# Kernel optimization log

Hardware: AMD Instinct MI355X
Metric: run time of the kernel (lower is better)

The kernel has to match this reference:

```python
import jax, jax.numpy as jnp
import numpy as np

N_NODES = 1024
FEAT = 64
NEG_BIG = -9e15

def setup_inputs() -> dict:
    key = jax.random.key(0)
    ks = jax.random.split(key, 12)
    B, S, D = 4, 16384, FEAT
    flow_features = jax.random.normal(ks[0], (B, S, D), dtype=jnp.float32)
    src_ips = jax.random.randint(ks[1], (B, S), 0, N_NODES)
    dst_ips = jax.random.randint(ks[2], (B, S), 0, N_NODES)
    flow_volumes = jax.random.uniform(ks[3], (B, S), dtype=jnp.float32) * 2000.0
    emb = jax.random.normal(ks[4], (N_NODES, D), dtype=jnp.float32) * 0.02
    We1 = jax.random.normal(ks[5], (2 * D, 32), dtype=jnp.float32) * 0.1
    be1 = jnp.zeros((32,), dtype=jnp.float32)
    We2 = jax.random.normal(ks[6], (32, 1), dtype=jnp.float32) * 0.1
    be2 = jnp.zeros((1,), dtype=jnp.float32)
    W = jax.random.normal(ks[7], (D, D), dtype=jnp.float32) * 0.1
    a1 = jax.random.normal(ks[8], (D,), dtype=jnp.float32) * 0.1
    a2 = jax.random.normal(ks[9], (D,), dtype=jnp.float32) * 0.1
    return dict(flow_features=flow_features, src_ips=src_ips, dst_ips=dst_ips,
                flow_volumes=flow_volumes, emb=emb, We1=We1, be1=be1, We2=We2,
                be2=be2, W=W, a1=a1, a2=a2)

def _forward(flow_features, flow_volumes, emb, We1, be1, We2, be2, W, a1, a2,
             src_ips, dst_ips):
    B, S, D = flow_features.shape
    N = emb.shape[0]
    # --- DynamicGraphBuilder: scatter-add flow features at dst nodes ---
    node = jax.vmap(lambda f, d: jnp.zeros((N, D), f.dtype).at[d].add(f))(
        flow_features, dst_ips)                         # (B, N, D)
    nrm = jnp.maximum(jnp.linalg.norm(node, axis=-1, keepdims=True), 1e-12)
    h = node / nrm                                      # F.normalize(p=2)
    # --- edge weights: MLP over concat(src_emb, dst_emb), scaled by volume ---
    pair = jnp.concatenate([emb[src_ips], emb[dst_ips]], axis=-1)  # (B, S, 2D)
    mid = jax.nn.relu(pair @ We1 + be1)
    ew = jax.nn.sigmoid((mid @ We2 + be2)[..., 0])      # (B, S)
    w = ew * jax.nn.sigmoid(flow_volumes / 1000.0)
    adj = jax.vmap(lambda s, d, ww: jnp.zeros((N, N), ww.dtype)
                   .at[s, d].set(ww).at[d, s].set(ww))(src_ips, dst_ips, w)
    # --- GraphAttentionLayer (decomposed e_ij = a1.Wh_i + a2.Wh_j) ---
    Wh = h @ W                                          # (B, N, D)
    f1 = Wh @ a1                                        # (B, N)
    f2 = Wh @ a2                                        # (B, N)
    e = jax.nn.leaky_relu(f1[:, :, None] + f2[:, None, :], 0.2)  # (B, N, N)
    attn = jax.nn.softmax(jnp.where(adj > 0, e, NEG_BIG), axis=-1)
    return jax.nn.elu(jnp.einsum('bij,bjd->bid', attn, Wh))       # (B, N, D)

def reference(flow_features, src_ips, dst_ips, flow_volumes, emb, We1, be1,
              We2, be2, W, a1, a2):
    return _forward(flow_features, flow_volumes, emb, We1, be1, We2, be2,
                    W, a1, a2, src_ips, dst_ips)
```

## Files before the change

kernel.cpp:

```cpp
#include <hip/hip_runtime.h>
#include <math.h>

#define BB 4
#define SS 16384
#define NN 1024
#define DD 64
#define MW 32
#define CAP 256
#define JCAP 256

__device__ __forceinline__ float wave_sum(float v) {
    #pragma unroll
    for (int off = 32; off > 0; off >>= 1) v += __shfl_xor(v, off, 64);
    return v;
}
__device__ __forceinline__ float wave_max(float v) {
    #pragma unroll
    for (int off = 32; off > 0; off >>= 1) v = fmaxf(v, __shfl_xor(v, off, 64));
    return v;
}

__global__ __launch_bounds__(256) void build_kernel(
        const int* __restrict__ src_ips, const int* __restrict__ dst_ips,
        int* __restrict__ count, int* __restrict__ bucket,
        unsigned int* __restrict__ mask) {
    int tid = blockIdx.x * 256 + threadIdx.x;
    int b   = tid >> 14;
    int dst = dst_ips[tid];
    int src = src_ips[tid];
    int row = (b << 10) + dst;
    int pos = atomicAdd(count + row, 1);
    if (pos < CAP) bucket[row * CAP + pos] = tid;
    unsigned int* mb = mask + (size_t)b * NN * MW;
    atomicOr(mb + src * MW + (dst >> 5), 1u << (dst & 31));
    atomicOr(mb + dst * MW + (src >> 5), 1u << (src & 31));
}

__global__ __launch_bounds__(256) void gather_transform_kernel(
        const float* __restrict__ ff, const int* __restrict__ count,
        const int* __restrict__ bucket, const float* __restrict__ W,
        const float* __restrict__ a1, const float* __restrict__ a2,
        float* __restrict__ Wh, float* __restrict__ f1, float* __restrict__ f2) {
    __shared__ float Ws[DD * DD];
    __shared__ float hs[4][DD];
    __shared__ float a1s[DD], a2s[DD];
    int t = threadIdx.x;
    for (int i = t; i < DD * DD / 4; i += 256)
        ((float4*)Ws)[i] = ((const float4*)W)[i];
    if (t < DD) { a1s[t] = a1[t]; a2s[t] = a2[t]; }
    int wave = t >> 6, lane = t & 63;
    int fq = lane >> 4;
    int qi = lane & 15;
    int row = blockIdx.x * 4 + wave;

    int cnt = min(count[row], CAP);
    const int* bk = bucket + (size_t)row * CAP;
    int bkreg = (lane < cnt) ? bk[lane] : 0;
    float4 v = make_float4(0.f, 0.f, 0.f, 0.f);
    int lim = min(cnt, 64);
    for (int base = 0; base < lim; base += 4) {
        int fi = base + fq;
        int flow = __shfl(bkreg, fi, 64);
        if (fi < lim) {
            float4 x = ((const float4*)(ff + (size_t)flow * DD))[qi];
            v.x += x.x; v.y += x.y; v.z += x.z; v.w += x.w;
        }
    }
    for (int base = 64; base < cnt; base += 4) {
        int fi = base + fq;
        if (fi < cnt) {
            int flow = bk[fi];
            float4 x = ((const float4*)(ff + (size_t)flow * DD))[qi];
            v.x += x.x; v.y += x.y; v.z += x.z; v.w += x.w;
        }
    }
    #pragma unroll
    for (int off = 16; off <= 32; off <<= 1) {
        v.x += __shfl_xor(v.x, off, 64);
        v.y += __shfl_xor(v.y, off, 64);
        v.z += __shfl_xor(v.z, off, 64);
        v.w += __shfl_xor(v.w, off, 64);
    }
    float ssq = (fq == 0) ? (v.x*v.x + v.y*v.y + v.z*v.z + v.w*v.w) : 0.f;
    float nrm = fmaxf(sqrtf(wave_sum(ssq)), 1e-12f);
    float inv = 1.f / nrm;
    __syncthreads();
    if (fq == 0)
        ((float4*)hs[wave])[qi] = make_float4(v.x*inv, v.y*inv, v.z*inv, v.w*inv);
    float whl = 0.f;
    #pragma unroll
    for (int k = 0; k < DD; ++k)
        whl = fmaf(hs[wave][k], Ws[k * DD + lane], whl);
    Wh[row * DD + lane] = whl;
    float p1 = wave_sum(whl * a1s[lane]);
    float p2 = wave_sum(whl * a2s[lane]);
    if (lane == 0) { f1[row] = p1; f2[row] = p2; }
}

__global__ __launch_bounds__(256) void attn_kernel(
        const unsigned int* __restrict__ mask, const float* __restrict__ f1,
        const float* __restrict__ f2, const float* __restrict__ Wh,
        float* __restrict__ out) {
    __shared__ unsigned int ms[4][MW];
    __shared__ float ps[4][NN];
    __shared__ int   jls[4][JCAP];
    int t = threadIdx.x;
    int wave = t >> 6, lane = t & 63;
    int row = blockIdx.x * 4 + wave;
    int b = row >> 10;
    const unsigned int* mrow = mask + (size_t)row * MW;
    if (lane < MW) ms[wave][lane] = mrow[lane];
    __syncthreads();
    const float* f2b = f2 + b * NN;
    const float* Whb = Wh + (size_t)(b << 10) * DD;
    float f1i = f1[row];

    unsigned int mword = (lane < MW) ? ms[wave][lane] : 0u;
    int pc = __popc(mword);
    int x = pc;
    #pragma unroll
    for (int off = 1; off < 64; off <<= 1) {
        int y = __shfl_up(x, off, 64);
        if (lane >= off) x += y;
    }
    int cnt = __shfl(x, 63, 64);
    int o = x - pc;
    if (cnt <= JCAP) {
        unsigned int bits = mword;
        while (bits) {
            int bidx = __ffs(bits) - 1; bits &= bits - 1;
            jls[wave][o++] = (lane << 5) + bidx;
        }
    }
    __syncthreads();

    float ev[16];
    float m = -INFINITY;
    #pragma unroll
    for (int tt = 0; tt < 16; ++tt) {
        int j = lane + (tt << 6);
        ev[tt] = -INFINITY;
        if (ms[wave][j >> 5] & (1u << (j & 31))) {
            float e = f1i + f2b[j];
            ev[tt] = (e >= 0.f) ? e : 0.2f * e;
            m = fmaxf(m, ev[tt]);
        }
    }
    m = wave_max(m);
    float lsum = 0.f;
    #pragma unroll
    for (int tt = 0; tt < 16; ++tt) {
        float p = (ev[tt] > -INFINITY) ? __expf(ev[tt] - m) : 0.f;
        ps[wave][lane + (tt << 6)] = p;
        lsum += p;
    }
    lsum = wave_sum(lsum);

    float acc = 0.f;
    if (cnt > 0 && cnt <= JCAP) {
        const int* jl = jls[wave];
        int k = 0;
        for (; k + 4 <= cnt; k += 4) {
            int j0 = jl[k], j1 = jl[k+1], j2 = jl[k+2], j3 = jl[k+3];
            float w0 = Whb[j0 * DD + lane];
            float w1 = Whb[j1 * DD + lane];
            float w2 = Whb[j2 * DD + lane];
            float w3 = Whb[j3 * DD + lane];
            acc = fmaf(ps[wave][j0], w0, acc);
            acc = fmaf(ps[wave][j1], w1, acc);
            acc = fmaf(ps[wave][j2], w2, acc);
            acc = fmaf(ps[wave][j3], w3, acc);
        }
        for (; k < cnt; ++k) {
            int j = jl[k];
            acc = fmaf(ps[wave][j], Whb[j * DD + lane], acc);
        }
        acc /= lsum;
    } else if (cnt > JCAP) {
        for (int w = 0; w < MW; ++w) {
            unsigned int bits = ms[wave][w];
            while (bits) {
                int j = (w << 5) + (__ffs(bits) - 1);
                bits &= bits - 1;
                acc = fmaf(ps[wave][j], Whb[j * DD + lane], acc);
            }
        }
        acc /= lsum;
    } else {
        for (int j = 0; j < NN; ++j) acc += Whb[j * DD + lane];
        acc *= (1.f / NN);
    }
    out[row * DD + lane] = (acc > 0.f) ? acc : expm1f(acc);
}

extern "C" void kernel_launch(void* const* d_in, const int* in_sizes, int n_in,
                              void* d_out, int out_size, void* d_ws, size_t ws_size,
                              hipStream_t stream) {
    const float* ff      = (const float*)d_in[0];
    const int*   src_ips = (const int*)d_in[1];
    const int*   dst_ips = (const int*)d_in[2];
    const float* W  = (const float*)d_in[9];
    const float* a1 = (const float*)d_in[10];
    const float* a2 = (const float*)d_in[11];
    float* out = (float*)d_out;

    char* ws = (char*)d_ws;
    int* count         = (int*)ws;
    unsigned int* mask = (unsigned int*)(ws + (16 << 10));
    float* f1          = (float*)(ws + (528 << 10));
    float* f2          = (float*)(ws + (544 << 10));
    int* bucket        = (int*)(ws + (1 << 20));
    float* Wh          = (float*)(ws + (5 << 20));

    hipMemsetAsync(count, 0, (528 << 10), stream);

    build_kernel<<<BB * SS / 256, 256, 0, stream>>>(src_ips, dst_ips, count, bucket, mask);
    gather_transform_kernel<<<BB * NN / 4, 256, 0, stream>>>(ff, count, bucket, W, a1, a2, Wh, f1, f2);
    attn_kernel<<<BB * NN / 4, 256, 0, stream>>>(mask, f1, f2, Wh, out);
}
```

Measured before the change: 110.0 us.

## Compute softmax only over neighbor list and vectorize aggregation with float4 lanes

The attention kernel now computes scores, max and exp only for the compacted neighbor list instead of all 1024 columns, and stores probabilities in a small per-neighbor shared array. The weighted aggregation is reorganized so each quarter-wave handles a different neighbor, with float4 loads and a cross-quarter shuffle reduction. The mask word is kept in registers via shuffles, which removes the shared staging and both block barriers. The aim is to cut wasted exp and memory work on sparse rows, at the cost of recomputing f2 lookups twice and more code branches.

```diff
diff --git a/kernel.cpp b/kernel.cpp
--- a/kernel.cpp
+++ b/kernel.cpp
@@ -101,21 +101,17 @@
         const unsigned int* __restrict__ mask, const float* __restrict__ f1,
         const float* __restrict__ f2, const float* __restrict__ Wh,
         float* __restrict__ out) {
-    __shared__ unsigned int ms[4][MW];
-    __shared__ float ps[4][NN];
     __shared__ int   jls[4][JCAP];
+    __shared__ float pls[4][JCAP];
     int t = threadIdx.x;
     int wave = t >> 6, lane = t & 63;
     int row = blockIdx.x * 4 + wave;
     int b = row >> 10;
-    const unsigned int* mrow = mask + (size_t)row * MW;
-    if (lane < MW) ms[wave][lane] = mrow[lane];
-    __syncthreads();
+    unsigned int mword = (lane < MW) ? mask[(size_t)row * MW + lane] : 0u;
     const float* f2b = f2 + b * NN;
     const float* Whb = Wh + (size_t)(b << 10) * DD;
     float f1i = f1[row];
 
-    unsigned int mword = (lane < MW) ? ms[wave][lane] : 0u;
     int pc = __popc(mword);
     int x = pc;
     #pragma unroll
@@ -132,65 +128,117 @@
             jls[wave][o++] = (lane << 5) + bidx;
         }
     }
-    __syncthreads();
-
-    float ev[16];
-    float m = -INFINITY;
-    #pragma unroll
-    for (int tt = 0; tt < 16; ++tt) {
-        int j = lane + (tt << 6);
-        ev[tt] = -INFINITY;
-        if (ms[wave][j >> 5] & (1u << (j & 31))) {
+
+    int fq = lane >> 4;
+    int qi = lane & 15;
+
+    if (cnt > 0 && cnt <= JCAP) {
+        float m = -INFINITY;
+        for (int k = lane; k < cnt; k += 64) {
+            int j = jls[wave][k];
             float e = f1i + f2b[j];
-            ev[tt] = (e >= 0.f) ? e : 0.2f * e;
-            m = fmaxf(m, ev[tt]);
-        }
-    }
-    m = wave_max(m);
-    float lsum = 0.f;
-    #pragma unroll
-    for (int tt = 0; tt < 16; ++tt) {
-        float p = (ev[tt] > -INFINITY) ? __expf(ev[tt] - m) : 0.f;
-        ps[wave][lane + (tt << 6)] = p;
-        lsum += p;
-    }
-    lsum = wave_sum(lsum);
-
-    float acc = 0.f;
-    if (cnt > 0 && cnt <= JCAP) {
-        const int* jl = jls[wave];
-        int k = 0;
-        for (; k + 4 <= cnt; k += 4) {
-            int j0 = jl[k], j1 = jl[k+1], j2 = jl[k+2], j3 = jl[k+3];
-            float w0 = Whb[j0 * DD + lane];
-            float w1 = Whb[j1 * DD + lane];
-            float w2 = Whb[j2 * DD + lane];
-            float w3 = Whb[j3 * DD + lane];
-            acc = fmaf(ps[wave][j0], w0, acc);
-            acc = fmaf(ps[wave][j1], w1, acc);
-            acc = fmaf(ps[wave][j2], w2, acc);
-            acc = fmaf(ps[wave][j3], w3, acc);
-        }
-        for (; k < cnt; ++k) {
-            int j = jl[k];
-            acc = fmaf(ps[wave][j], Whb[j * DD + lane], acc);
-        }
-        acc /= lsum;
-    } else if (cnt > JCAP) {
+            e = (e >= 0.f) ? e : 0.2f * e;
+            m = fmaxf(m, e);
+        }
+        m = wave_max(m);
+        float lsum = 0.f;
+        for (int k = lane; k < cnt; k += 64) {
+            int j = jls[wave][k];
+            float e = f1i + f2b[j];
+            e = (e >= 0.f) ? e : 0.2f * e;
+            float p = __expf(e - m);
+            pls[wave][k] = p;
+            lsum += p;
+        }
+        lsum = wave_sum(lsum);
+        float4 acc = make_float4(0.f, 0.f, 0.f, 0.f);
+        for (int k = fq; k < cnt; k += 4) {
+            int j   = jls[wave][k];
+            float p = pls[wave][k];
+            float4 w = ((const float4*)(Whb + (size_t)j * DD))[qi];
+            acc.x = fmaf(p, w.x, acc.x);
+            acc.y = fmaf(p, w.y, acc.y);
+            acc.z = fmaf(p, w.z, acc.z);
+            acc.w = fmaf(p, w.w, acc.w);
+        }
+        #pragma unroll
+        for (int off = 16; off <= 32; off <<= 1) {
+            acc.x += __shfl_xor(acc.x, off, 64);
+            acc.y += __shfl_xor(acc.y, off, 64);
+            acc.z += __shfl_xor(acc.z, off, 64);
+            acc.w += __shfl_xor(acc.w, off, 64);
+        }
+        if (fq == 0) {
+            float inv = 1.f / lsum;
+            float4 r;
+            r.x = acc.x * inv; r.y = acc.y * inv;
+            r.z = acc.z * inv; r.w = acc.w * inv;
+            r.x = (r.x > 0.f) ? r.x : expm1f(r.x);
+            r.y = (r.y > 0.f) ? r.y : expm1f(r.y);
+            r.z = (r.z > 0.f) ? r.z : expm1f(r.z);
+            r.w = (r.w > 0.f) ? r.w : expm1f(r.w);
+            ((float4*)(out + (size_t)row * DD))[qi] = r;
+        }
+    } else if (cnt == 0) {
+        float4 acc = make_float4(0.f, 0.f, 0.f, 0.f);
+        for (int k = fq; k < NN; k += 4) {
+            float4 w = ((const float4*)(Whb + (size_t)k * DD))[qi];
+            acc.x += w.x; acc.y += w.y; acc.z += w.z; acc.w += w.w;
+        }
+        #pragma unroll
+        for (int off = 16; off <= 32; off <<= 1) {
+            acc.x += __shfl_xor(acc.x, off, 64);
+            acc.y += __shfl_xor(acc.y, off, 64);
+            acc.z += __shfl_xor(acc.z, off, 64);
+            acc.w += __shfl_xor(acc.w, off, 64);
+        }
+        if (fq == 0) {
+            float4 r;
+            r.x = acc.x * (1.f / NN); r.y = acc.y * (1.f / NN);
+            r.z = acc.z * (1.f / NN); r.w = acc.w * (1.f / NN);
+            r.x = (r.x > 0.f) ? r.x : expm1f(r.x);
+            r.y = (r.y > 0.f) ? r.y : expm1f(r.y);
+            r.z = (r.z > 0.f) ? r.z : expm1f(r.z);
+            r.w = (r.w > 0.f) ? r.w : expm1f(r.w);
+            ((float4*)(out + (size_t)row * DD))[qi] = r;
+        }
+    } else {
+        float m = -INFINITY;
+        for (int tt = 0; tt < 16; ++tt) {
+            int j = lane + (tt << 6);
+            unsigned int wv = __shfl(mword, j >> 5, 64);
+            if (wv & (1u << (j & 31))) {
+                float e = f1i + f2b[j];
+                e = (e >= 0.f) ? e : 0.2f * e;
+                m = fmaxf(m, e);
+            }
+        }
+        m = wave_max(m);
+        float lsum = 0.f;
+        for (int tt = 0; tt < 16; ++tt) {
+            int j = lane + (tt << 6);
+            unsigned int wv = __shfl(mword, j >> 5, 64);
+            if (wv & (1u << (j & 31))) {
+                float e = f1i + f2b[j];
+                e = (e >= 0.f) ? e : 0.2f * e;
+                lsum += __expf(e - m);
+            }
+        }
+        lsum = wave_sum(lsum);
+        float acc = 0.f;
         for (int w = 0; w < MW; ++w) {
-            unsigned int bits = ms[wave][w];
+            unsigned int bits = __shfl(mword, w, 64);
             while (bits) {
                 int j = (w << 5) + (__ffs(bits) - 1);
                 bits &= bits - 1;
-                acc = fmaf(ps[wave][j], Whb[j * DD + lane], acc);
+                float e = f1i + f2b[j];
+                e = (e >= 0.f) ? e : 0.2f * e;
+                acc = fmaf(__expf(e - m), Whb[(size_t)j * DD + lane], acc);
             }
         }
         acc /= lsum;
-    } else {
-        for (int j = 0; j < NN; ++j) acc += Whb[j * DD + lane];
-        acc *= (1.f / NN);
-    }
-    out[row * DD + lane] = (acc > 0.f) ? acc : expm1f(acc);
+        out[(size_t)row * DD + lane] = (acc > 0.f) ? acc : expm1f(acc);
+    }
 }
 
 extern "C" void kernel_launch(void* const* d_in, const int* in_sizes, int n_in,
```

Result: no change. 108.2 us (-1.7%).
